# Optimization experiments

Measured on AMD Instinct MI355X. Metric: run time of the kernel, lower is better.

## Reference

```python
import jax, jax.numpy as jnp
import numpy as np

N, F, D, H, E = 100000, 256, 128, 4, 1000000
C = D // H  # out_channels per head


def setup_inputs() -> dict:
    key = jax.random.key(0)
    ks = jax.random.split(key, 10)
    glorot = lambda k, shp, fan: jax.random.normal(k, shp, jnp.float32) * (2.0 / sum(fan)) ** 0.5
    return {
        "x": jax.random.normal(ks[0], (N, F), jnp.float32),
        "edge_index_0": jax.random.randint(ks[1], (2, E), 0, N, jnp.int32),
        "edge_index_1": jax.random.randint(ks[2], (2, E), 0, N, jnp.int32),
        "W_lin": glorot(ks[3], (F, D), (F, D)),
        "b_lin": jnp.zeros((D,), jnp.float32),
        "attn_l": glorot(ks[4], (2, H, C), (H, C)),
        "attn_r": glorot(ks[5], (2, H, C), (H, C)),
        "alpha_act": jnp.ones((2,), jnp.float32),  # 'sharpening' init 1.0
        "W_conv": glorot(ks[6], (3, F), (F, 3)),
        "b_conv": jnp.zeros((3,), jnp.float32),
    }


def _segment_softmax(a, seg, n):
    # a: [E, H], seg: [E] destination indices
    amax = jax.ops.segment_max(a, seg, num_segments=n)  # [N, H], -inf for empty segs
    ex = jnp.exp(a - amax[seg])
    denom = jax.ops.segment_sum(ex, seg, num_segments=n)
    return ex / denom[seg]


def reference(x, edge_index_0, edge_index_1, W_lin, b_lin, attn_l, attn_r, alpha_act, W_conv, b_conv):
    # get_h_dict: Linear(F -> D) then reshape [N, H, C]
    h = x @ W_lin + b_lin                      # [N, D]
    hh = h.reshape(N, H, C)
    # get_beta_weights: Conv1d(F, 3, kernel_size=1) on x.unsqueeze(-1) == linear per node; softmax over relations
    beta = jax.nn.softmax(x @ W_conv.T + b_conv, axis=1)  # [N, 3]

    # agg_relation_neighbors: per-metapath GAT-style attention + scatter-add
    rel_outs = []
    for m, ei in enumerate((edge_index_0, edge_index_1)):
        al = jnp.sum(hh * attn_l[m], axis=-1)  # [N, H]
        ar = jnp.sum(hh * attn_r[m], axis=-1)  # [N, H]
        dst, src_j = ei[0], ei[1]              # flow target_to_source: aggregate at edge_index[0]
        a = (ar[src_j] + al[dst]) * alpha_act[m]   # message alpha_j + alpha_i, sharpening activation
        alpha = _segment_softmax(a, dst, N)        # softmax per destination node
        msg = hh[src_j] * alpha[:, :, None]        # [E, H, C]
        rel_outs.append(jax.ops.segment_sum(msg, dst, num_segments=N).reshape(N, D))
    # last relation slot holds the node's own h (first=True)
    emb = jnp.stack(rel_outs + [h], axis=1)        # [N, 3, D]
    out = jnp.einsum('nrd,nr->nd', emb, beta)      # matmul(emb^T, beta).squeeze(-1)
    return jax.nn.relu(out)                        # embedding_activation 'relu'
```

## Files before the change

kernel.cpp:

```cpp
#include <hip/hip_runtime.h>
#include <hip/hip_bf16.h>

#define NN 100000
#define FF 256
#define DD 128
#define EE 1000000

typedef __attribute__((ext_vector_type(4))) float f32x4;
typedef __attribute__((ext_vector_type(8))) short bf16x8;

__device__ __forceinline__ ushort f2bf(float f) {
    __hip_bfloat16 h = __float2bfloat16(f);
    return *reinterpret_cast<ushort*>(&h);
}
__device__ __forceinline__ float bf2f(ushort u) {
    return __uint_as_float(((uint)u) << 16);
}

__global__ void pack_w(const float* __restrict__ Wl, ushort* __restrict__ Wt) {
    int id = blockIdx.x * 256 + threadIdx.x;
    int k = id >> 7, n = id & 127;
    Wt[n * FF + k] = f2bf(Wl[id]);
}

__global__ __launch_bounds__(256) void fused_h(const float* __restrict__ x,
                                               const ushort* __restrict__ Wt,
                                               const float* __restrict__ bl,
                                               const float* __restrict__ Wc,
                                               const float* __restrict__ bc,
                                               ushort* __restrict__ hb,
                                               float* __restrict__ beta) {
    __shared__ ushort xs[64][72];
    __shared__ ushort wsT[128][72];
    __shared__ ushort hs[64][136];
    __shared__ float wcs[768];

    int t = threadIdx.x;
    int wv = t >> 6, lane = t & 63;
    int row0 = blockIdx.x * 64;
    int br = t >> 2, bq = t & 3;
    bool rowok = (row0 + br) < NN;

    if (t < 192) ((float4*)wcs)[t] = ((const float4*)Wc)[t];
    __syncthreads();

    f32x4 acc[8];
    #pragma unroll
    for (int i = 0; i < 8; ++i) acc[i] = (f32x4){0.f, 0.f, 0.f, 0.f};

    float bs0 = 0.f, bs1 = 0.f, bs2 = 0.f;

    for (int k0 = 0; k0 < FF; k0 += 64) {
        if (rowok) {
            const float4* xp = (const float4*)(x + (size_t)(row0 + br) * FF + k0 + bq * 16);
            #pragma unroll
            for (int j = 0; j < 4; ++j) {
                float4 v = xp[j];
                int kk = bq * 16 + j * 4;
                const float* w0 = wcs + k0 + kk;
                bs0 += v.x * w0[0] + v.y * w0[1] + v.z * w0[2] + v.w * w0[3];
                const float* w1 = wcs + 256 + k0 + kk;
                bs1 += v.x * w1[0] + v.y * w1[1] + v.z * w1[2] + v.w * w1[3];
                const float* w2 = wcs + 512 + k0 + kk;
                bs2 += v.x * w2[0] + v.y * w2[1] + v.z * w2[2] + v.w * w2[3];
                ushort4 p;
                p.x = f2bf(v.x); p.y = f2bf(v.y); p.z = f2bf(v.z); p.w = f2bf(v.w);
                *(ushort4*)&xs[br][kk] = p;
            }
        } else {
            ushort4 z = {0, 0, 0, 0};
            #pragma unroll
            for (int j = 0; j < 4; ++j) *(ushort4*)&xs[br][bq * 16 + j * 4] = z;
        }
        #pragma unroll
        for (int j = 0; j < 4; ++j) {
            int c = t + 256 * j;
            int rw = c >> 3, seg = c & 7;
            uint4 v = *(const uint4*)(Wt + rw * FF + k0 + seg * 8);
            *(uint4*)&wsT[rw][seg * 8] = v;
        }
        __syncthreads();
        #pragma unroll
        for (int ks = 0; ks < 2; ++ks) {
            bf16x8 af = *(const bf16x8*)&xs[wv * 16 + (lane & 15)][ks * 32 + (lane >> 4) * 8];
            #pragma unroll
            for (int nt = 0; nt < 8; ++nt) {
                bf16x8 bv = *(const bf16x8*)&wsT[nt * 16 + (lane & 15)][ks * 32 + (lane >> 4) * 8];
                acc[nt] = __builtin_amdgcn_mfma_f32_16x16x32_bf16(af, bv, acc[nt], 0, 0, 0);
            }
        }
        __syncthreads();
    }

    bs0 += __shfl_xor(bs0, 1); bs0 += __shfl_xor(bs0, 2);
    bs1 += __shfl_xor(bs1, 1); bs1 += __shfl_xor(bs1, 2);
    bs2 += __shfl_xor(bs2, 1); bs2 += __shfl_xor(bs2, 2);
    if (bq == 0 && rowok) {
        float s0 = bs0 + bc[0], s1 = bs1 + bc[1], s2 = bs2 + bc[2];
        float mx = fmaxf(s0, fmaxf(s1, s2));
        float e0 = __expf(s0 - mx), e1 = __expf(s1 - mx), e2 = __expf(s2 - mx);
        float inv = 1.f / (e0 + e1 + e2);
        int n = row0 + br;
        beta[n * 3 + 0] = e0 * inv;
        beta[n * 3 + 1] = e1 * inv;
        beta[n * 3 + 2] = e2 * inv;
    }

    #pragma unroll
    for (int nt = 0; nt < 8; ++nt) {
        int col = nt * 16 + (lane & 15);
        float bias = bl[col];
        int rbase = wv * 16 + (lane >> 4) * 4;
        #pragma unroll
        for (int r = 0; r < 4; ++r) {
            hs[rbase + r][col] = f2bf(acc[nt][r] + bias);
        }
    }
    __syncthreads();
    #pragma unroll
    for (int j = 0; j < 4; ++j) {
        int c = t + 256 * j;
        int rw = c >> 4, seg = c & 15;
        if (row0 + rw < NN) {
            uint4 v = *(const uint4*)&hs[rw][seg * 8];
            *(uint4*)(hb + (size_t)(row0 + rw) * DD + seg * 8) = v;
        }
    }
}

__global__ __launch_bounds__(256) void alr_kernel(const ushort* __restrict__ hb,
                                                  const float* __restrict__ attn_l,
                                                  const float* __restrict__ attn_r,
                                                  float* __restrict__ AL,
                                                  float* __restrict__ AR) {
    int wid = threadIdx.x >> 6, lane = threadIdx.x & 63;
    int n = blockIdx.x * 4 + wid;
    uint hv = ((const uint*)hb)[(size_t)n * 64 + lane];
    float hx = bf2f((ushort)(hv & 0xffff)), hy = bf2f((ushort)(hv >> 16));
    int hd = lane >> 4;
    int cg = lane & 15;
    #pragma unroll
    for (int m = 0; m < 2; ++m) {
        float2 wl = ((const float2*)attn_l)[m * 64 + hd * 16 + cg];
        float2 wr = ((const float2*)attn_r)[m * 64 + hd * 16 + cg];
        float sl = hx * wl.x + hy * wl.y;
        float sr = hx * wr.x + hy * wr.y;
        for (int off = 1; off < 16; off <<= 1) {
            sl += __shfl_xor(sl, off);
            sr += __shfl_xor(sr, off);
        }
        if (cg == 0) {
            AL[(size_t)(m * NN + n) * 4 + hd] = sl;
            AR[(size_t)(m * NN + n) * 4 + hd] = sr;
        }
    }
}

__global__ void count_kernel(const int* __restrict__ ei0, const int* __restrict__ ei1,
                             int* __restrict__ deg) {
    int e = blockIdx.x * 256 + threadIdx.x;
    if (e < EE) {
        atomicAdd(&deg[ei0[e]], 1);
    } else if (e < 2 * EE) {
        atomicAdd(&deg[NN + ei1[e - EE]], 1);
    }
}

__global__ __launch_bounds__(256) void scan1(const int* __restrict__ deg, int* __restrict__ rp,
                                             int* __restrict__ bsum, int L) {
    __shared__ int sm[256];
    int t = threadIdx.x;
    int i = blockIdx.x * 256 + t;
    int v = (i < L) ? deg[i] : 0;
    sm[t] = v;
    __syncthreads();
    for (int off = 1; off < 256; off <<= 1) {
        int o = (t >= off) ? sm[t - off] : 0;
        __syncthreads();
        sm[t] += o;
        __syncthreads();
    }
    if (i < L) rp[i] = sm[t] - v;
    if (t == 255) bsum[blockIdx.x] = sm[255];
}

__global__ __launch_bounds__(256) void scan2(int* __restrict__ bsum, int nb) {
    __shared__ int sm[256];
    int t = threadIdx.x;
    int carry = 0;
    for (int base = 0; base < nb; base += 256) {
        int i = base + t;
        int v = (i < nb) ? bsum[i] : 0;
        __syncthreads();
        sm[t] = v;
        __syncthreads();
        for (int off = 1; off < 256; off <<= 1) {
            int o = (t >= off) ? sm[t - off] : 0;
            __syncthreads();
            sm[t] += o;
            __syncthreads();
        }
        int incl = sm[t];
        int tot = sm[255];
        if (i < nb) bsum[i] = carry + incl - v;
        carry += tot;
    }
}

__global__ void scan3(int* __restrict__ rp, const int* __restrict__ bsum, int L) {
    int i = blockIdx.x * 256 + threadIdx.x;
    if (i < L) rp[i] += bsum[blockIdx.x];
    if (i == 0) rp[L] = 2 * EE;
}

__global__ void scatter_kernel(const int* __restrict__ ei0, const int* __restrict__ ei1,
                               const int* __restrict__ rp, int* __restrict__ cursor,
                               int* __restrict__ srcs) {
    int e = blockIdx.x * 256 + threadIdx.x;
    int idx, src;
    if (e < EE) {
        idx = ei0[e];
        src = ei0[EE + e];
    } else if (e < 2 * EE) {
        int e1 = e - EE;
        idx = NN + ei1[e1];
        src = ei1[EE + e1];
    } else {
        return;
    }
    int pos = rp[idx] + atomicAdd(&cursor[idx], 1);
    srcs[pos] = src;
}

__global__ __launch_bounds__(256) void main_kernel(const ushort* __restrict__ hb,
                                                   const float* __restrict__ AL,
                                                   const float* __restrict__ AR,
                                                   const float* __restrict__ beta,
                                                   const float* __restrict__ alpha_act,
                                                   const int* __restrict__ rp,
                                                   const int* __restrict__ srcs,
                                                   float* __restrict__ out) {
    int wid = threadIdx.x >> 6, lane = threadIdx.x & 63;
    int n = blockIdx.x * 4 + wid;
    const uint* h2 = (const uint*)hb;
    uint hv = h2[(size_t)n * 64 + lane];
    float hx = bf2f((ushort)(hv & 0xffff)), hy = bf2f((ushort)(hv >> 16));
    int hd = lane >> 4;
    float b0 = beta[n * 3 + 0], b1 = beta[n * 3 + 1], b2 = beta[n * 3 + 2];
    float ox = b2 * hx, oy = b2 * hy;
    float bm[2] = {b0, b1};
    #pragma unroll
    for (int m = 0; m < 2; ++m) {
        float alv = AL[(size_t)(m * NN + n) * 4 + hd];
        float am = alpha_act[m];
        int e0 = rp[m * NN + n];
        int e1 = rp[m * NN + n + 1];
        float denom = 0.f, ax = 0.f, ay = 0.f;
        int e = e0;
        for (; e + 4 <= e1; e += 4) {
            int s0 = srcs[e + 0], s1 = srcs[e + 1], s2 = srcs[e + 2], s3 = srcs[e + 3];
            float r0 = AR[(size_t)(m * NN + s0) * 4 + hd];
            float r1 = AR[(size_t)(m * NN + s1) * 4 + hd];
            float r2 = AR[(size_t)(m * NN + s2) * 4 + hd];
            float r3 = AR[(size_t)(m * NN + s3) * 4 + hd];
            uint g0 = h2[(size_t)s0 * 64 + lane];
            uint g1 = h2[(size_t)s1 * 64 + lane];
            uint g2 = h2[(size_t)s2 * 64 + lane];
            uint g3 = h2[(size_t)s3 * 64 + lane];
            float p0 = __expf((r0 + alv) * am);
            float p1 = __expf((r1 + alv) * am);
            float p2 = __expf((r2 + alv) * am);
            float p3 = __expf((r3 + alv) * am);
            denom += (p0 + p1) + (p2 + p3);
            ax += p0 * bf2f((ushort)(g0 & 0xffff)) + p1 * bf2f((ushort)(g1 & 0xffff))
                + p2 * bf2f((ushort)(g2 & 0xffff)) + p3 * bf2f((ushort)(g3 & 0xffff));
            ay += p0 * bf2f((ushort)(g0 >> 16)) + p1 * bf2f((ushort)(g1 >> 16))
                + p2 * bf2f((ushort)(g2 >> 16)) + p3 * bf2f((ushort)(g3 >> 16));
        }
        for (; e < e1; ++e) {
            int s = srcs[e];
            float rv = AR[(size_t)(m * NN + s) * 4 + hd];
            float p = __expf((rv + alv) * am);
            denom += p;
            uint g = h2[(size_t)s * 64 + lane];
            ax += p * bf2f((ushort)(g & 0xffff));
            ay += p * bf2f((ushort)(g >> 16));
        }
        float invd = (denom > 0.f) ? (1.f / denom) : 0.f;
        ox += bm[m] * ax * invd;
        oy += bm[m] * ay * invd;
    }
    float2 res;
    res.x = fmaxf(ox, 0.f);
    res.y = fmaxf(oy, 0.f);
    ((float2*)out)[(size_t)n * 64 + lane] = res;
}

extern "C" void kernel_launch(void* const* d_in, const int* in_sizes, int n_in,
                              void* d_out, int out_size, void* d_ws, size_t ws_size,
                              hipStream_t stream) {
    const float* x      = (const float*)d_in[0];
    const int*   ei0    = (const int*)d_in[1];
    const int*   ei1    = (const int*)d_in[2];
    const float* W_lin  = (const float*)d_in[3];
    const float* b_lin  = (const float*)d_in[4];
    const float* attn_l = (const float*)d_in[5];
    const float* attn_r = (const float*)d_in[6];
    const float* alpha  = (const float*)d_in[7];
    const float* W_conv = (const float*)d_in[8];
    const float* b_conv = (const float*)d_in[9];
    float* out = (float*)d_out;

    char* ws = (char*)d_ws;
    size_t off = 0;
    ushort* hb   = (ushort*)(ws + off); off += (size_t)NN * DD * 2;
    ushort* Wt   = (ushort*)(ws + off); off += (size_t)DD * FF * 2;
    float* AL    = (float*)(ws + off);  off += (size_t)2 * NN * 4 * 4;
    float* AR    = (float*)(ws + off);  off += (size_t)2 * NN * 4 * 4;
    float* beta  = (float*)(ws + off);  off += (size_t)NN * 3 * 4;
    int*   deg   = (int*)(ws + off);    off += (size_t)2 * NN * 4;
    int*   cursor= (int*)(ws + off);    off += (size_t)2 * NN * 4;
    int*   rp    = (int*)(ws + off);    off += ((size_t)2 * NN + 4) * 4;
    int*   bsum  = (int*)(ws + off);    off += 1024 * 4;
    int*   srcs  = (int*)(ws + off);    off += (size_t)2 * EE * 4;

    hipMemsetAsync(deg, 0, (size_t)4 * NN * 4, stream);

    pack_w<<<DD * FF / 256, 256, 0, stream>>>(W_lin, Wt);
    fused_h<<<(NN + 63) / 64, 256, 0, stream>>>(x, Wt, b_lin, W_conv, b_conv, hb, beta);
    alr_kernel<<<NN / 4, 256, 0, stream>>>(hb, attn_l, attn_r, AL, AR);
    count_kernel<<<(2 * EE + 255) / 256, 256, 0, stream>>>(ei0, ei1, deg);
    int L = 2 * NN;
    int nb = (L + 255) / 256;
    scan1<<<nb, 256, 0, stream>>>(deg, rp, bsum, L);
    scan2<<<1, 256, 0, stream>>>(bsum, nb);
    scan3<<<nb, 256, 0, stream>>>(rp, bsum, L);
    scatter_kernel<<<(2 * EE + 255) / 256, 256, 0, stream>>>(ei0, ei1, rp, cursor, srcs);
    main_kernel<<<NN / 4, 256, 0, stream>>>(hb, AL, AR, beta, alpha, rp, srcs, out);
}
```

Measured before the change: 385.6 us.

## Partition edge atomics by destination range and split relations across waves

Count and scatter kernels now use 1024 blocks. Each block scans a chunk of edges but only does atomics for destinations in one of eight node ranges, with the aim of keeping atomic targets localized per XCD/L2. Because every edge is read eight times, edge-index read traffic rises eightfold. The main kernel assigns one wave per (node, relation) pair instead of one wave looping over both relations, doubling wave-level parallelism. It also replaces the scalar tail loop with clamped, masked 4-wide gathers. The two partial results are combined through shared memory with a block barrier.

```diff
diff --git a/kernel.cpp b/kernel.cpp
--- a/kernel.cpp
+++ b/kernel.cpp
@@ -5,6 +5,9 @@
 #define FF 256
 #define DD 128
 #define EE 1000000
+#define NPX (NN / 8)
+#define PART_BLOCKS 1024
+#define PART_CHUNK ((2 * EE) / (PART_BLOCKS / 8))
 
 typedef __attribute__((ext_vector_type(4))) float f32x4;
 typedef __attribute__((ext_vector_type(8))) short bf16x8;
@@ -156,13 +159,39 @@
     }
 }
 
-__global__ void count_kernel(const int* __restrict__ ei0, const int* __restrict__ ei1,
-                             int* __restrict__ deg) {
-    int e = blockIdx.x * 256 + threadIdx.x;
-    if (e < EE) {
-        atomicAdd(&deg[ei0[e]], 1);
-    } else if (e < 2 * EE) {
-        atomicAdd(&deg[NN + ei1[e - EE]], 1);
+__global__ __launch_bounds__(256) void count_kernel(const int* __restrict__ ei0,
+                                                    const int* __restrict__ ei1,
+                                                    int* __restrict__ deg) {
+    int b = blockIdx.x;
+    int lo = (b & 7) * NPX, hi = lo + NPX;
+    int e0 = (b >> 3) * PART_CHUNK;
+    for (int i = threadIdx.x; i < PART_CHUNK; i += 256) {
+        int e = e0 + i;
+        int dst, base;
+        if (e < EE) { dst = ei0[e]; base = 0; }
+        else        { dst = ei1[e - EE]; base = NN; }
+        if (dst >= lo && dst < hi) atomicAdd(&deg[base + dst], 1);
+    }
+}
+
+__global__ __launch_bounds__(256) void scatter_kernel(const int* __restrict__ ei0,
+                                                      const int* __restrict__ ei1,
+                                                      const int* __restrict__ rp,
+                                                      int* __restrict__ cursor,
+                                                      int* __restrict__ srcs) {
+    int b = blockIdx.x;
+    int lo = (b & 7) * NPX, hi = lo + NPX;
+    int e0 = (b >> 3) * PART_CHUNK;
+    for (int i = threadIdx.x; i < PART_CHUNK; i += 256) {
+        int e = e0 + i;
+        int dst, src, base;
+        if (e < EE) { dst = ei0[e]; src = ei0[EE + e]; base = 0; }
+        else        { int ee = e - EE; dst = ei1[ee]; src = ei1[EE + ee]; base = NN; }
+        if (dst >= lo && dst < hi) {
+            int idx = base + dst;
+            int pos = rp[idx] + atomicAdd(&cursor[idx], 1);
+            srcs[pos] = src;
+        }
     }
 }
 
@@ -213,25 +242,6 @@
     if (i == 0) rp[L] = 2 * EE;
 }
 
-__global__ void scatter_kernel(const int* __restrict__ ei0, const int* __restrict__ ei1,
-                               const int* __restrict__ rp, int* __restrict__ cursor,
-                               int* __restrict__ srcs) {
-    int e = blockIdx.x * 256 + threadIdx.x;
-    int idx, src;
-    if (e < EE) {
-        idx = ei0[e];
-        src = ei0[EE + e];
-    } else if (e < 2 * EE) {
-        int e1 = e - EE;
-        idx = NN + ei1[e1];
-        src = ei1[EE + e1];
-    } else {
-        return;
-    }
-    int pos = rp[idx] + atomicAdd(&cursor[idx], 1);
-    srcs[pos] = src;
-}
-
 __global__ __launch_bounds__(256) void main_kernel(const ushort* __restrict__ hb,
                                                    const float* __restrict__ AL,
                                                    const float* __restrict__ AR,
@@ -240,60 +250,63 @@
                                                    const int* __restrict__ rp,
                                                    const int* __restrict__ srcs,
                                                    float* __restrict__ out) {
-    int wid = threadIdx.x >> 6, lane = threadIdx.x & 63;
-    int n = blockIdx.x * 4 + wid;
+    __shared__ float2 contribs[2][64];
+    int w = threadIdx.x >> 6, lane = threadIdx.x & 63;
+    int slot = w >> 1, m = w & 1;
+    int n = blockIdx.x * 2 + slot;
     const uint* h2 = (const uint*)hb;
-    uint hv = h2[(size_t)n * 64 + lane];
-    float hx = bf2f((ushort)(hv & 0xffff)), hy = bf2f((ushort)(hv >> 16));
     int hd = lane >> 4;
-    float b0 = beta[n * 3 + 0], b1 = beta[n * 3 + 1], b2 = beta[n * 3 + 2];
-    float ox = b2 * hx, oy = b2 * hy;
-    float bm[2] = {b0, b1};
-    #pragma unroll
-    for (int m = 0; m < 2; ++m) {
-        float alv = AL[(size_t)(m * NN + n) * 4 + hd];
-        float am = alpha_act[m];
-        int e0 = rp[m * NN + n];
-        int e1 = rp[m * NN + n + 1];
-        float denom = 0.f, ax = 0.f, ay = 0.f;
-        int e = e0;
-        for (; e + 4 <= e1; e += 4) {
-            int s0 = srcs[e + 0], s1 = srcs[e + 1], s2 = srcs[e + 2], s3 = srcs[e + 3];
-            float r0 = AR[(size_t)(m * NN + s0) * 4 + hd];
-            float r1 = AR[(size_t)(m * NN + s1) * 4 + hd];
-            float r2 = AR[(size_t)(m * NN + s2) * 4 + hd];
-            float r3 = AR[(size_t)(m * NN + s3) * 4 + hd];
-            uint g0 = h2[(size_t)s0 * 64 + lane];
-            uint g1 = h2[(size_t)s1 * 64 + lane];
-            uint g2 = h2[(size_t)s2 * 64 + lane];
-            uint g3 = h2[(size_t)s3 * 64 + lane];
-            float p0 = __expf((r0 + alv) * am);
-            float p1 = __expf((r1 + alv) * am);
-            float p2 = __expf((r2 + alv) * am);
-            float p3 = __expf((r3 + alv) * am);
-            denom += (p0 + p1) + (p2 + p3);
-            ax += p0 * bf2f((ushort)(g0 & 0xffff)) + p1 * bf2f((ushort)(g1 & 0xffff))
-                + p2 * bf2f((ushort)(g2 & 0xffff)) + p3 * bf2f((ushort)(g3 & 0xffff));
-            ay += p0 * bf2f((ushort)(g0 >> 16)) + p1 * bf2f((ushort)(g1 >> 16))
-                + p2 * bf2f((ushort)(g2 >> 16)) + p3 * bf2f((ushort)(g3 >> 16));
-        }
-        for (; e < e1; ++e) {
-            int s = srcs[e];
-            float rv = AR[(size_t)(m * NN + s) * 4 + hd];
-            float p = __expf((rv + alv) * am);
-            denom += p;
-            uint g = h2[(size_t)s * 64 + lane];
-            ax += p * bf2f((ushort)(g & 0xffff));
-            ay += p * bf2f((ushort)(g >> 16));
-        }
-        float invd = (denom > 0.f) ? (1.f / denom) : 0.f;
-        ox += bm[m] * ax * invd;
-        oy += bm[m] * ay * invd;
-    }
-    float2 res;
-    res.x = fmaxf(ox, 0.f);
-    res.y = fmaxf(oy, 0.f);
-    ((float2*)out)[(size_t)n * 64 + lane] = res;
+
+    float alv = AL[(size_t)(m * NN + n) * 4 + hd];
+    float am = alpha_act[m];
+    float bm = beta[n * 3 + m];
+    int e0 = rp[m * NN + n];
+    int e1 = rp[m * NN + n + 1];
+    const float* ARm = AR + (size_t)m * NN * 4;
+
+    float denom = 0.f, ax = 0.f, ay = 0.f;
+    for (int e = e0; e < e1; e += 4) {
+        int last = e1 - 1;
+        int i1 = min(e + 1, last), i2 = min(e + 2, last), i3 = min(e + 3, last);
+        int s0 = srcs[e], s1 = srcs[i1], s2 = srcs[i2], s3 = srcs[i3];
+        float r0 = ARm[s0 * 4 + hd];
+        float r1 = ARm[s1 * 4 + hd];
+        float r2 = ARm[s2 * 4 + hd];
+        float r3 = ARm[s3 * 4 + hd];
+        uint g0 = h2[(size_t)s0 * 64 + lane];
+        uint g1 = h2[(size_t)s1 * 64 + lane];
+        uint g2 = h2[(size_t)s2 * 64 + lane];
+        uint g3 = h2[(size_t)s3 * 64 + lane];
+        float v1 = (e + 1 < e1) ? 1.f : 0.f;
+        float v2 = (e + 2 < e1) ? 1.f : 0.f;
+        float v3 = (e + 3 < e1) ? 1.f : 0.f;
+        float p0 = __expf((r0 + alv) * am);
+        float p1 = v1 * __expf((r1 + alv) * am);
+        float p2 = v2 * __expf((r2 + alv) * am);
+        float p3 = v3 * __expf((r3 + alv) * am);
+        denom += (p0 + p1) + (p2 + p3);
+        ax += p0 * bf2f((ushort)(g0 & 0xffff)) + p1 * bf2f((ushort)(g1 & 0xffff))
+            + p2 * bf2f((ushort)(g2 & 0xffff)) + p3 * bf2f((ushort)(g3 & 0xffff));
+        ay += p0 * bf2f((ushort)(g0 >> 16)) + p1 * bf2f((ushort)(g1 >> 16))
+            + p2 * bf2f((ushort)(g2 >> 16)) + p3 * bf2f((ushort)(g3 >> 16));
+    }
+    float invd = (denom > 0.f) ? (1.f / denom) : 0.f;
+    float cx = bm * ax * invd;
+    float cy = bm * ay * invd;
+
+    if (m == 1) contribs[slot][lane] = make_float2(cx, cy);
+    __syncthreads();
+    if (m == 0) {
+        uint hv = h2[(size_t)n * 64 + lane];
+        float b2 = beta[n * 3 + 2];
+        float2 c1 = contribs[slot][lane];
+        float ox = b2 * bf2f((ushort)(hv & 0xffff)) + cx + c1.x;
+        float oy = b2 * bf2f((ushort)(hv >> 16)) + cy + c1.y;
+        float2 res;
+        res.x = fmaxf(ox, 0.f);
+        res.y = fmaxf(oy, 0.f);
+        ((float2*)out)[(size_t)n * 64 + lane] = res;
+    }
 }
 
 extern "C" void kernel_launch(void* const* d_in, const int* in_sizes, int n_in,
@@ -329,12 +342,12 @@
     pack_w<<<DD * FF / 256, 256, 0, stream>>>(W_lin, Wt);
     fused_h<<<(NN + 63) / 64, 256, 0, stream>>>(x, Wt, b_lin, W_conv, b_conv, hb, beta);
     alr_kernel<<<NN / 4, 256, 0, stream>>>(hb, attn_l, attn_r, AL, AR);
-    count_kernel<<<(2 * EE + 255) / 256, 256, 0, stream>>>(ei0, ei1, deg);
+    count_kernel<<<PART_BLOCKS, 256, 0, stream>>>(ei0, ei1, deg);
     int L = 2 * NN;
     int nb = (L + 255) / 256;
     scan1<<<nb, 256, 0, stream>>>(deg, rp, bsum, L);
     scan2<<<1, 256, 0, stream>>>(bsum, nb);
     scan3<<<nb, 256, 0, stream>>>(rp, bsum, L);
-    scatter_kernel<<<(2 * EE + 255) / 256, 256, 0, stream>>>(ei0, ei1, rp, cursor, srcs);
-    main_kernel<<<NN / 4, 256, 0, stream>>>(hb, AL, AR, beta, alpha, rp, srcs, out);
-}
+    scatter_kernel<<<PART_BLOCKS, 256, 0, stream>>>(ei0, ei1, rp, cursor, srcs);
+    main_kernel<<<NN / 2, 256, 0, stream>>>(hb, AL, AR, beta, alpha, rp, srcs, out);
+}
```

Result: faster. 354.8 us (-8.0%).
